# Kernel optimization log

Hardware: AMD Instinct MI355X
Metric: run time of the kernel (lower is better)

## Reference

```python
import jax, jax.numpy as jnp
import numpy as np

D = 1024
H = 16
HD = D // H


def setup_inputs() -> dict:
    key = jax.random.key(0)
    ks = jax.random.split(key, 5)
    s = 1.0 / np.sqrt(D)
    return {
        "inputs": jax.random.normal(ks[0], (2, 2048, D), dtype=jnp.float32),
        "Wq": jax.random.normal(ks[1], (D, D), dtype=jnp.float32) * s,
        "bq": jnp.zeros((D,), jnp.float32),
        "Wk": jax.random.normal(ks[2], (D, D), dtype=jnp.float32) * s,
        "bk": jnp.zeros((D,), jnp.float32),
        "Wv": jax.random.normal(ks[3], (D, D), dtype=jnp.float32) * s,
        "bv": jnp.zeros((D,), jnp.float32),
        "Wo": jax.random.normal(ks[4], (D, D), dtype=jnp.float32) * s,
        "bo": jnp.zeros((D,), jnp.float32),
    }


def reference(inputs, Wq, bq, Wk, bk, Wv, bv, Wo, bo):
    B, S, _ = inputs.shape
    def split_heads(x):  # [B,S,D] -> [B,H,S,hd]
        return x.reshape(B, S, H, HD).transpose(0, 2, 1, 3)
    q = split_heads(inputs @ Wq + bq)
    k = split_heads(inputs @ Wk + bk)
    v = split_heads(inputs @ Wv + bv)
    scale = 1.0 / jnp.sqrt(jnp.asarray(HD, inputs.dtype))
    scores = jnp.einsum("bhsd,bhtd->bhst", q, k) * scale  # [B,H,S,S]
    weights = jax.nn.softmax(scores, axis=-1)
    attn = jnp.einsum("bhst,bhtd->bhsd", weights, v)
    concat = attn.transpose(0, 2, 1, 3).reshape(B, S, D)
    return concat @ Wo + bo
```

## Files before the change

kernel.cpp:

```cpp
#include <hip/hip_runtime.h>


typedef __bf16 bf16x8 __attribute__((ext_vector_type(8)));
typedef float  f32x4  __attribute__((ext_vector_type(4)));

#if __has_builtin(__builtin_amdgcn_exp2f)
#define EXPFN(x) __builtin_amdgcn_exp2f(x)
#define QSCALE (0.125f * 1.44269504088896f)
#else
#define EXPFN(x) __expf(x)
#define QSCALE 0.125f
#endif

#define LDKP 74

__device__ __forceinline__ unsigned short f2bf(float f) {
    unsigned int u = __float_as_uint(f);
    u += 0x7FFFu + ((u >> 16) & 1u);
    return (unsigned short)(u >> 16);
}

__device__ __forceinline__ void gload16(const void* g, void* l) {
    __builtin_amdgcn_global_load_lds(
        (const __attribute__((address_space(1))) void*)g,
        (__attribute__((address_space(3))) void*)l, 16, 0, 0);
}

#define WAIT0_BARRIER() asm volatile("s_waitcnt vmcnt(0)\n\ts_barrier" ::: "memory")

__global__ __launch_bounds__(256) void prep_kernel(
    const float* __restrict__ X, ushort4* __restrict__ Xb,
    const float* __restrict__ Wq, const float* __restrict__ Wk,
    const float* __restrict__ Wv, const float* __restrict__ Wo,
    unsigned short* __restrict__ Wt_all) {
    const int z = blockIdx.z;
    if (z == 4) {
        int base = (blockIdx.y * 32 + blockIdx.x) * 1024 + threadIdx.x;
        const float4* X4 = (const float4*)X;
        #pragma unroll
        for (int c = 0; c < 4; c++) {
            int i = base + c * 256;
            float4 v = X4[i];
            ushort4 o;
            o.x = f2bf(v.x); o.y = f2bf(v.y); o.z = f2bf(v.z); o.w = f2bf(v.w);
            Xb[i] = o;
        }
        return;
    }
    __shared__ float tile[32][33];
    const float* W = (z == 0) ? Wq : (z == 1) ? Wk : (z == 2) ? Wv : Wo;
    unsigned short* Wt = Wt_all + (size_t)z * 1024 * 1024;
    int c0 = blockIdx.x * 32, r0 = blockIdx.y * 32;
    int x = threadIdx.x & 31, y = threadIdx.x >> 5;
    for (int j = 0; j < 32; j += 8)
        tile[y + j][x] = W[(r0 + y + j) * 1024 + c0 + x];
    __syncthreads();
    for (int j = 0; j < 32; j += 8)
        Wt[(c0 + y + j) * 1024 + r0 + x] = f2bf(tile[x][y + j]);
}

__global__ __launch_bounds__(256) void gemm_qkv_kernel(
    const unsigned short* __restrict__ Xb, const unsigned short* __restrict__ Wt_all,
    const float* __restrict__ bq, const float* __restrict__ bk,
    const float* __restrict__ bv,
    unsigned short* __restrict__ Qb, unsigned short* __restrict__ Kb,
    unsigned short* __restrict__ Vt) {
    const int z = blockIdx.z;
    const int x0 = blockIdx.x * 128;
    const int y0 = blockIdx.y * 128;

    const unsigned short* Ap;
    const unsigned short* Bp;
    if (z < 2) {
        Ap = Xb + (size_t)x0 * 1024;
        Bp = Wt_all + (size_t)z * 1024 * 1024 + (size_t)y0 * 1024;
    } else {
        Ap = Wt_all + (size_t)2 * 1024 * 1024 + (size_t)y0 * 1024;
        Bp = Xb + (size_t)x0 * 1024;
    }

    __shared__ __align__(16) unsigned short As[2][128 * 64];
    __shared__ __align__(16) unsigned short Bs[2][128 * 64];

    const int tid = threadIdx.x;
    const int lane = tid & 63, wave = tid >> 6;
    const int quad = lane >> 4, l15 = lane & 15;
    const int wrow = (wave >> 1) * 64, wcol = (wave & 1) * 64;

    f32x4 acc[4][4] = {};

    const int srow = lane >> 3;
    const int ch8  = (lane & 7) * 8;
    const int swz  = (((lane & 7) ^ srow)) * 8;
    const int sw   = (l15 & 7);

    #pragma unroll
    for (int c = 0; c < 4; c++) {
        int r = c * 32 + wave * 8 + srow;
        gload16(Ap + (size_t)r * 1024 + 0 + swz, &As[0][r * 64 + ch8]);
        gload16(Bp + (size_t)r * 1024 + 0 + swz, &Bs[0][r * 64 + ch8]);
    }

    for (int k = 0; k < 16; k++) {
        const int cur = k & 1, nxt = cur ^ 1;
        WAIT0_BARRIER();
        if (k < 15) {
            int k0 = (k + 1) * 64;
            #pragma unroll
            for (int c = 0; c < 4; c++) {
                int r = c * 32 + wave * 8 + srow;
                gload16(Ap + (size_t)r * 1024 + k0 + swz, &As[nxt][r * 64 + ch8]);
                gload16(Bp + (size_t)r * 1024 + k0 + swz, &Bs[nxt][r * 64 + ch8]);
            }
        }
        #pragma unroll
        for (int kk = 0; kk < 2; kk++) {
            bf16x8 af[4], bfr[4];
            #pragma unroll
            for (int i = 0; i < 4; i++)
                af[i] = *(const bf16x8*)&As[cur][(wrow + i * 16 + l15) * 64 +
                                                (((kk * 4 + quad) ^ sw)) * 8];
            #pragma unroll
            for (int j = 0; j < 4; j++)
                bfr[j] = *(const bf16x8*)&Bs[cur][(wcol + j * 16 + l15) * 64 +
                                                 (((kk * 4 + quad) ^ sw)) * 8];
            #pragma unroll
            for (int i = 0; i < 4; i++)
                #pragma unroll
                for (int j = 0; j < 4; j++)
                    acc[i][j] = __builtin_amdgcn_mfma_f32_16x16x32_bf16(
                        af[i], bfr[j], acc[i][j], 0, 0, 0);
        }
    }

    if (z < 2) {
        const float* bias = (z == 0) ? bq : bk;
        #pragma unroll
        for (int j = 0; j < 4; j++) {
            int col = y0 + wcol + j * 16 + l15;
            float bcol = bias[col];
            int h = col >> 6, d = col & 63;
            #pragma unroll
            for (int i = 0; i < 4; i++)
                #pragma unroll
                for (int r = 0; r < 4; r++) {
                    int row = x0 + wrow + i * 16 + quad * 4 + r;
                    int b = row >> 11, s = row & 2047;
                    float v = acc[i][j][r] + bcol;
                    if (z == 0)
                        Qb[(size_t)((b * 16 + h) * 2048 + s) * 64 + d] = f2bf(v * QSCALE);
                    else
                        Kb[(size_t)((b * 16 + h) * 2048 + s) * 64 + d] = f2bf(v);
                }
        }
    } else {
        #pragma unroll
        for (int i = 0; i < 4; i++)
            #pragma unroll
            for (int r = 0; r < 4; r++) {
                int rowd = y0 + wrow + i * 16 + quad * 4 + r;
                float brow = bv[rowd];
                #pragma unroll
                for (int j = 0; j < 4; j++) {
                    int colm = x0 + wcol + j * 16 + l15;
                    int b = colm >> 11, s = colm & 2047;
                    Vt[(size_t)(b * 1024 + rowd) * 2048 + s] = f2bf(acc[i][j][r] + brow);
                }
            }
    }
}

__global__ __launch_bounds__(256) void attn_kernel(
    const unsigned short* __restrict__ Qb, const unsigned short* __restrict__ Kb,
    const unsigned short* __restrict__ Vt, unsigned short* __restrict__ Cc,
    float* __restrict__ Op, float* __restrict__ Lp, int tlen, int do_split) {
    const int bh = blockIdx.y;
    const int b = bh >> 4, h = bh & 15;
    const int q0 = blockIdx.x * 128;
    const int split = blockIdx.z;
    const int tbeg = split * tlen;

    const int tid = threadIdx.x;
    const int lane = tid & 63, wave = tid >> 6;
    const int quad = lane >> 4, l15 = lane & 15;

    __shared__ __align__(16) unsigned short Ks[2][64 * 64];
    __shared__ __align__(16) unsigned short Vs[2][64 * 64];
    __shared__ __align__(16) unsigned short Ps[4][32 * LDKP];

    const unsigned short* Qbh = Qb + (size_t)bh * 2048 * 64;
    const unsigned short* Kbh = Kb + (size_t)bh * 2048 * 64;
    const unsigned short* Vbh = Vt + (size_t)bh * 64 * 2048;

    bf16x8 qa[2][2];
    #pragma unroll
    for (int mi = 0; mi < 2; mi++)
        #pragma unroll
        for (int kk = 0; kk < 2; kk++)
            qa[mi][kk] = *(const bf16x8*)&Qbh[
                (size_t)(q0 + wave * 32 + mi * 16 + l15) * 64 + kk * 32 + quad * 8];

    union { unsigned short us[8]; bf16x8 v; } ones_u;
    #pragma unroll
    for (int i = 0; i < 8; i++) ones_u.us[i] = 0x3F80;
    const bf16x8 onesv = ones_u.v;

    f32x4 o[2][4] = {};
    f32x4 ol[2] = {};

    const int srow = lane >> 3;
    const int r0s = wave * 16 + srow;
    const int ch8 = (lane & 7) * 8;
    const int swz = (((lane & 7) ^ srow)) * 8;
    const int sw  = (l15 & 7);

    {
        const int t0 = tbeg;
        gload16(&Kbh[(size_t)(t0 + r0s) * 64 + swz],       &Ks[0][r0s * 64 + ch8]);
        gload16(&Kbh[(size_t)(t0 + r0s + 8) * 64 + swz],   &Ks[0][(r0s + 8) * 64 + ch8]);
        gload16(&Vbh[(size_t)r0s * 2048 + t0 + swz],       &Vs[0][r0s * 64 + ch8]);
        gload16(&Vbh[(size_t)(r0s + 8) * 2048 + t0 + swz], &Vs[0][(r0s + 8) * 64 + ch8]);
    }

    const int niter = tlen >> 6;
    for (int it = 0; it < niter; it++) {
        const int cur = it & 1, nxt = cur ^ 1;
        WAIT0_BARRIER();
        if (it + 1 < niter) {
            const int t0 = tbeg + (it + 1) * 64;
            gload16(&Kbh[(size_t)(t0 + r0s) * 64 + swz],       &Ks[nxt][r0s * 64 + ch8]);
            gload16(&Kbh[(size_t)(t0 + r0s + 8) * 64 + swz],   &Ks[nxt][(r0s + 8) * 64 + ch8]);
            gload16(&Vbh[(size_t)r0s * 2048 + t0 + swz],       &Vs[nxt][r0s * 64 + ch8]);
            gload16(&Vbh[(size_t)(r0s + 8) * 2048 + t0 + swz], &Vs[nxt][(r0s + 8) * 64 + ch8]);
        }

        f32x4 sf[2][4] = {};
        #pragma unroll
        for (int j = 0; j < 4; j++)
            #pragma unroll
            for (int kk = 0; kk < 2; kk++) {
                bf16x8 kf = *(const bf16x8*)&Ks[cur][(j * 16 + l15) * 64 +
                                                     (((kk * 4 + quad) ^ sw)) * 8];
                sf[0][j] = __builtin_amdgcn_mfma_f32_16x16x32_bf16(qa[0][kk], kf, sf[0][j], 0, 0, 0);
                sf[1][j] = __builtin_amdgcn_mfma_f32_16x16x32_bf16(qa[1][kk], kf, sf[1][j], 0, 0, 0);
            }

        #pragma unroll
        for (int mi = 0; mi < 2; mi++)
            #pragma unroll
            for (int j = 0; j < 4; j++)
                #pragma unroll
                for (int r = 0; r < 4; r++) {
                    float p = EXPFN(sf[mi][j][r]);
                    Ps[wave][(mi * 16 + quad * 4 + r) * LDKP + j * 16 + l15] =
                        (unsigned short)(__float_as_uint(p) >> 16);
                }

        asm volatile("s_waitcnt lgkmcnt(0)" ::: "memory");

        #pragma unroll
        for (int kk = 0; kk < 2; kk++) {
            bf16x8 pf0 = *(const bf16x8*)&Ps[wave][(l15) * LDKP + kk * 32 + quad * 8];
            bf16x8 pf1 = *(const bf16x8*)&Ps[wave][(16 + l15) * LDKP + kk * 32 + quad * 8];
            ol[0] = __builtin_amdgcn_mfma_f32_16x16x32_bf16(pf0, onesv, ol[0], 0, 0, 0);
            ol[1] = __builtin_amdgcn_mfma_f32_16x16x32_bf16(pf1, onesv, ol[1], 0, 0, 0);
            #pragma unroll
            for (int j = 0; j < 4; j++) {
                bf16x8 vf = *(const bf16x8*)&Vs[cur][(j * 16 + l15) * 64 +
                                                     (((kk * 4 + quad) ^ sw)) * 8];
                o[0][j] = __builtin_amdgcn_mfma_f32_16x16x32_bf16(pf0, vf, o[0][j], 0, 0, 0);
                o[1][j] = __builtin_amdgcn_mfma_f32_16x16x32_bf16(pf1, vf, o[1][j], 0, 0, 0);
            }
        }
    }

    if (do_split) {
        float* Opd = Op + (size_t)(split * 32 + bh) * 2048 * 64;
        float* Lpd = Lp + (size_t)(split * 32 + bh) * 2048;
        #pragma unroll
        for (int mi = 0; mi < 2; mi++)
            #pragma unroll
            for (int r = 0; r < 4; r++) {
                int s = q0 + wave * 32 + mi * 16 + quad * 4 + r;
                if (l15 == 0) Lpd[s] = ol[mi][r];
                #pragma unroll
                for (int j = 0; j < 4; j++)
                    Opd[(size_t)s * 64 + j * 16 + l15] = o[mi][j][r];
            }
    } else {
        #pragma unroll
        for (int mi = 0; mi < 2; mi++)
            #pragma unroll
            for (int r = 0; r < 4; r++) {
                float inv = 1.f / ol[mi][r];
                int s = q0 + wave * 32 + mi * 16 + quad * 4 + r;
                size_t row = (size_t)(b * 2048 + s);
                #pragma unroll
                for (int j = 0; j < 4; j++)
                    Cc[row * 1024 + h * 64 + j * 16 + l15] = f2bf(o[mi][j][r] * inv);
            }
    }
}

__global__ __launch_bounds__(256) void combine_kernel(
    const float4* __restrict__ Op, const float* __restrict__ Lp,
    unsigned short* __restrict__ Cc) {
    int idx = blockIdx.x * 256 + threadIdx.x;
    int d4 = idx & 15;
    int s = (idx >> 4) & 2047;
    int bh = idx >> 15;
    const size_t half4 = (size_t)32 * 2048 * 16;
    float4 a = Op[(size_t)idx], c = Op[half4 + (size_t)idx];
    float l = Lp[bh * 2048 + s] + Lp[32 * 2048 + bh * 2048 + s];
    float inv = 1.f / l;
    ushort4 o;
    o.x = f2bf((a.x + c.x) * inv); o.y = f2bf((a.y + c.y) * inv);
    o.z = f2bf((a.z + c.z) * inv); o.w = f2bf((a.w + c.w) * inv);
    int b = bh >> 4, h = bh & 15;
    *(ushort4*)&Cc[((size_t)(b * 2048 + s)) * 1024 + h * 64 + d4 * 4] = o;
}

__global__ __launch_bounds__(256) void gemm_out_kernel(
    const unsigned short* __restrict__ Cc, const unsigned short* __restrict__ Wot,
    const float* __restrict__ bo, float* __restrict__ out) {
    const int m0 = blockIdx.x * 128;
    const int n0 = blockIdx.y * 128;

    __shared__ __align__(16) unsigned short As[2][128 * 64];
    __shared__ __align__(16) unsigned short Bs[2][128 * 64];

    const int tid = threadIdx.x;
    const int lane = tid & 63, wave = tid >> 6;
    const int quad = lane >> 4, l15 = lane & 15;
    const int wrow = (wave >> 1) * 64, wcol = (wave & 1) * 64;

    f32x4 acc[4][4] = {};
    const int srow = lane >> 3;
    const int ch8 = (lane & 7) * 8;
    const int swz = (((lane & 7) ^ srow)) * 8;
    const int sw  = (l15 & 7);

    #pragma unroll
    for (int c = 0; c < 4; c++) {
        int r = c * 32 + wave * 8 + srow;
        gload16(Cc + (size_t)(m0 + r) * 1024 + swz,  &As[0][r * 64 + ch8]);
        gload16(Wot + (size_t)(n0 + r) * 1024 + swz, &Bs[0][r * 64 + ch8]);
    }

    for (int k = 0; k < 16; k++) {
        const int cur = k & 1, nxt = cur ^ 1;
        WAIT0_BARRIER();
        if (k < 15) {
            int k0 = (k + 1) * 64;
            #pragma unroll
            for (int c = 0; c < 4; c++) {
                int r = c * 32 + wave * 8 + srow;
                gload16(Cc + (size_t)(m0 + r) * 1024 + k0 + swz,  &As[nxt][r * 64 + ch8]);
                gload16(Wot + (size_t)(n0 + r) * 1024 + k0 + swz, &Bs[nxt][r * 64 + ch8]);
            }
        }
        #pragma unroll
        for (int kk = 0; kk < 2; kk++) {
            bf16x8 af[4], bfr[4];
            #pragma unroll
            for (int i = 0; i < 4; i++)
                af[i] = *(const bf16x8*)&As[cur][(wrow + i * 16 + l15) * 64 +
                                                (((kk * 4 + quad) ^ sw)) * 8];
            #pragma unroll
            for (int j = 0; j < 4; j++)
                bfr[j] = *(const bf16x8*)&Bs[cur][(wcol + j * 16 + l15) * 64 +
                                                 (((kk * 4 + quad) ^ sw)) * 8];
            #pragma unroll
            for (int i = 0; i < 4; i++)
                #pragma unroll
                for (int j = 0; j < 4; j++)
                    acc[i][j] = __builtin_amdgcn_mfma_f32_16x16x32_bf16(
                        af[i], bfr[j], acc[i][j], 0, 0, 0);
        }
    }

    #pragma unroll
    for (int j = 0; j < 4; j++) {
        int col = n0 + wcol + j * 16 + l15;
        float bcol = bo[col];
        #pragma unroll
        for (int i = 0; i < 4; i++)
            #pragma unroll
            for (int r = 0; r < 4; r++) {
                int row = m0 + wrow + i * 16 + quad * 4 + r;
                out[(size_t)row * 1024 + col] = acc[i][j][r] + bcol;
            }
    }
}

extern "C" void kernel_launch(void* const* d_in, const int* in_sizes, int n_in,
                              void* d_out, int out_size, void* d_ws, size_t ws_size,
                              hipStream_t stream) {
    const float* X  = (const float*)d_in[0];
    const float* Wq = (const float*)d_in[1];
    const float* bq = (const float*)d_in[2];
    const float* Wk = (const float*)d_in[3];
    const float* bk = (const float*)d_in[4];
    const float* Wv = (const float*)d_in[5];
    const float* bv = (const float*)d_in[6];
    const float* Wo = (const float*)d_in[7];
    const float* bo = (const float*)d_in[8];
    float* out = (float*)d_out;

    char* ws = (char*)d_ws;
    unsigned short* Xb = (unsigned short*)(ws);
    unsigned short* Wt = (unsigned short*)(ws + (8u  << 20));
    unsigned short* Qb = (unsigned short*)(ws + (16u << 20));
    unsigned short* Kb = (unsigned short*)(ws + (24u << 20));
    unsigned short* Vt = (unsigned short*)(ws + (32u << 20));
    unsigned short* Cc = (unsigned short*)(ws + (40u << 20));
    float* Op = (float*)(ws + (48u << 20));
    float* Lp = (float*)(ws + (48u << 20) + 33554432u);
    const bool use_split = ws_size >= ((size_t)(48u << 20) + 33554432u + 524288u);

    prep_kernel<<<dim3(32, 32, 5), 256, 0, stream>>>(X, (ushort4*)Xb, Wq, Wk, Wv, Wo, Wt);
    gemm_qkv_kernel<<<dim3(32, 8, 3), 256, 0, stream>>>(Xb, Wt, bq, bk, bv, Qb, Kb, Vt);
    if (use_split) {
        attn_kernel<<<dim3(16, 32, 2), 256, 0, stream>>>(Qb, Kb, Vt, Cc, Op, Lp, 1024, 1);
        combine_kernel<<<4096, 256, 0, stream>>>((const float4*)Op, Lp, Cc);
    } else {
        attn_kernel<<<dim3(16, 32, 1), 256, 0, stream>>>(Qb, Kb, Vt, Cc, Op, Lp, 2048, 0);
    }
    gemm_out_kernel<<<dim3(32, 8), 256, 0, stream>>>(Cc, Wt + 3u * 1024 * 1024, bo, out);
}
```

Measured before the change: 217.7 us.

## Drop LDS double buffering in GEMMs and halve output GEMM N tile

Both the QKV and the output projection GEMMs go from a double-buffered LDS prefetch pipeline to a single buffer: load, wait, compute, barrier. This halves LDS use per block to raise occupancy. The output GEMM also shrinks its N tile from 128 to 64, doubling the grid to 512 blocks to fill more CUs. The cost is that global loads no longer overlap MFMA work within a block, so latency hiding now depends on other resident blocks, and each step gains an extra barrier.

```diff
diff --git a/kernel.cpp b/kernel.cpp
--- a/kernel.cpp
+++ b/kernel.cpp
@@ -79,8 +79,8 @@
         Bp = Xb + (size_t)x0 * 1024;
     }
 
-    __shared__ __align__(16) unsigned short As[2][128 * 64];
-    __shared__ __align__(16) unsigned short Bs[2][128 * 64];
+    __shared__ __align__(16) unsigned short As[128 * 64];
+    __shared__ __align__(16) unsigned short Bs[128 * 64];
 
     const int tid = threadIdx.x;
     const int lane = tid & 63, wave = tid >> 6;
@@ -94,36 +94,25 @@
     const int swz  = (((lane & 7) ^ srow)) * 8;
     const int sw   = (l15 & 7);
 
-    #pragma unroll
-    for (int c = 0; c < 4; c++) {
-        int r = c * 32 + wave * 8 + srow;
-        gload16(Ap + (size_t)r * 1024 + 0 + swz, &As[0][r * 64 + ch8]);
-        gload16(Bp + (size_t)r * 1024 + 0 + swz, &Bs[0][r * 64 + ch8]);
-    }
-
-    for (int k = 0; k < 16; k++) {
-        const int cur = k & 1, nxt = cur ^ 1;
+    for (int k0 = 0; k0 < 1024; k0 += 64) {
+        #pragma unroll
+        for (int c = 0; c < 4; c++) {
+            int r = c * 32 + wave * 8 + srow;
+            gload16(Ap + (size_t)r * 1024 + k0 + swz, &As[r * 64 + ch8]);
+            gload16(Bp + (size_t)r * 1024 + k0 + swz, &Bs[r * 64 + ch8]);
+        }
         WAIT0_BARRIER();
-        if (k < 15) {
-            int k0 = (k + 1) * 64;
-            #pragma unroll
-            for (int c = 0; c < 4; c++) {
-                int r = c * 32 + wave * 8 + srow;
-                gload16(Ap + (size_t)r * 1024 + k0 + swz, &As[nxt][r * 64 + ch8]);
-                gload16(Bp + (size_t)r * 1024 + k0 + swz, &Bs[nxt][r * 64 + ch8]);
-            }
-        }
         #pragma unroll
         for (int kk = 0; kk < 2; kk++) {
             bf16x8 af[4], bfr[4];
             #pragma unroll
             for (int i = 0; i < 4; i++)
-                af[i] = *(const bf16x8*)&As[cur][(wrow + i * 16 + l15) * 64 +
-                                                (((kk * 4 + quad) ^ sw)) * 8];
+                af[i] = *(const bf16x8*)&As[(wrow + i * 16 + l15) * 64 +
+                                            (((kk * 4 + quad) ^ sw)) * 8];
             #pragma unroll
             for (int j = 0; j < 4; j++)
-                bfr[j] = *(const bf16x8*)&Bs[cur][(wcol + j * 16 + l15) * 64 +
-                                                 (((kk * 4 + quad) ^ sw)) * 8];
+                bfr[j] = *(const bf16x8*)&Bs[(wcol + j * 16 + l15) * 64 +
+                                             (((kk * 4 + quad) ^ sw)) * 8];
             #pragma unroll
             for (int i = 0; i < 4; i++)
                 #pragma unroll
@@ -131,6 +120,7 @@
                     acc[i][j] = __builtin_amdgcn_mfma_f32_16x16x32_bf16(
                         af[i], bfr[j], acc[i][j], 0, 0, 0);
         }
+        __syncthreads();
     }
 
     if (z < 2) {
@@ -324,63 +314,54 @@
     const unsigned short* __restrict__ Cc, const unsigned short* __restrict__ Wot,
     const float* __restrict__ bo, float* __restrict__ out) {
     const int m0 = blockIdx.x * 128;
-    const int n0 = blockIdx.y * 128;
-
-    __shared__ __align__(16) unsigned short As[2][128 * 64];
-    __shared__ __align__(16) unsigned short Bs[2][128 * 64];
+    const int n0 = blockIdx.y * 64;
+
+    __shared__ __align__(16) unsigned short As[128 * 64];
+    __shared__ __align__(16) unsigned short Bs[64 * 64];
 
     const int tid = threadIdx.x;
     const int lane = tid & 63, wave = tid >> 6;
     const int quad = lane >> 4, l15 = lane & 15;
-    const int wrow = (wave >> 1) * 64, wcol = (wave & 1) * 64;
-
-    f32x4 acc[4][4] = {};
+    const int wrow = (wave >> 1) * 64, wcol = (wave & 1) * 32;
+
+    f32x4 acc[4][2] = {};
     const int srow = lane >> 3;
     const int ch8 = (lane & 7) * 8;
     const int swz = (((lane & 7) ^ srow)) * 8;
     const int sw  = (l15 & 7);
 
-    #pragma unroll
-    for (int c = 0; c < 4; c++) {
-        int r = c * 32 + wave * 8 + srow;
-        gload16(Cc + (size_t)(m0 + r) * 1024 + swz,  &As[0][r * 64 + ch8]);
-        gload16(Wot + (size_t)(n0 + r) * 1024 + swz, &Bs[0][r * 64 + ch8]);
-    }
-
-    for (int k = 0; k < 16; k++) {
-        const int cur = k & 1, nxt = cur ^ 1;
+    for (int k0 = 0; k0 < 1024; k0 += 64) {
+        #pragma unroll
+        for (int c = 0; c < 4; c++) {
+            int r = c * 32 + wave * 8 + srow;
+            gload16(Cc + (size_t)(m0 + r) * 1024 + k0 + swz, &As[r * 64 + ch8]);
+            if (c < 2)
+                gload16(Wot + (size_t)(n0 + r) * 1024 + k0 + swz, &Bs[r * 64 + ch8]);
+        }
         WAIT0_BARRIER();
-        if (k < 15) {
-            int k0 = (k + 1) * 64;
-            #pragma unroll
-            for (int c = 0; c < 4; c++) {
-                int r = c * 32 + wave * 8 + srow;
-                gload16(Cc + (size_t)(m0 + r) * 1024 + k0 + swz,  &As[nxt][r * 64 + ch8]);
-                gload16(Wot + (size_t)(n0 + r) * 1024 + k0 + swz, &Bs[nxt][r * 64 + ch8]);
-            }
-        }
         #pragma unroll
         for (int kk = 0; kk < 2; kk++) {
-            bf16x8 af[4], bfr[4];
+            bf16x8 af[4], bfr[2];
             #pragma unroll
             for (int i = 0; i < 4; i++)
-                af[i] = *(const bf16x8*)&As[cur][(wrow + i * 16 + l15) * 64 +
-                                                (((kk * 4 + quad) ^ sw)) * 8];
-            #pragma unroll
-            for (int j = 0; j < 4; j++)
-                bfr[j] = *(const bf16x8*)&Bs[cur][(wcol + j * 16 + l15) * 64 +
-                                                 (((kk * 4 + quad) ^ sw)) * 8];
+                af[i] = *(const bf16x8*)&As[(wrow + i * 16 + l15) * 64 +
+                                            (((kk * 4 + quad) ^ sw)) * 8];
+            #pragma unroll
+            for (int j = 0; j < 2; j++)
+                bfr[j] = *(const bf16x8*)&Bs[(wcol + j * 16 + l15) * 64 +
+                                             (((kk * 4 + quad) ^ sw)) * 8];
             #pragma unroll
             for (int i = 0; i < 4; i++)
                 #pragma unroll
-                for (int j = 0; j < 4; j++)
+                for (int j = 0; j < 2; j++)
                     acc[i][j] = __builtin_amdgcn_mfma_f32_16x16x32_bf16(
                         af[i], bfr[j], acc[i][j], 0, 0, 0);
         }
+        __syncthreads();
     }
 
     #pragma unroll
-    for (int j = 0; j < 4; j++) {
+    for (int j = 0; j < 2; j++) {
         int col = n0 + wcol + j * 16 + l15;
         float bcol = bo[col];
         #pragma unroll
@@ -426,5 +407,5 @@
     } else {
         attn_kernel<<<dim3(16, 32, 1), 256, 0, stream>>>(Qb, Kb, Vt, Cc, Op, Lp, 2048, 0);
     }
-    gemm_out_kernel<<<dim3(32, 8), 256, 0, stream>>>(Cc, Wt + 3u * 1024 * 1024, bo, out);
-}
+    gemm_out_kernel<<<dim3(32, 16), 256, 0, stream>>>(Cc, Wt + 3u * 1024 * 1024, bo, out);
+}
```

Result: faster. 208.3 us (-4.3%).
